# Kernel optimization log

Measured on AMD Instinct MI355X. Metric: run time of the kernel, lower is better.

## Reference

```python
import jax, jax.numpy as jnp
import numpy as np
from jax import lax


def setup_inputs() -> dict:
    key = jax.random.key(0)
    k1, k2 = jax.random.split(key)
    B, T, C = 8, 4096, 256
    UNITS, WINDOW = 256, 2
    x = jax.random.normal(k1, (B, T, C), dtype=jnp.float32)
    kernel = jax.random.normal(k2, (WINDOW, C, 3 * UNITS), dtype=jnp.float32) * 0.05
    bias = jnp.zeros((3 * UNITS,), dtype=jnp.float32)
    return {"x": x, "kernel": kernel, "bias": bias}


def _qrnn_forward(x, kernel, bias):
    # Causal conv1d: left-pad time axis by (window - 1).
    window = kernel.shape[0]
    xp = jnp.pad(x, ((0, 0), (window - 1, 0), (0, 0)))
    gates = lax.conv_general_dilated(
        xp, kernel, window_strides=(1,), padding='VALID',
        dimension_numbers=('NWC', 'WIO', 'NWC')) + bias
    z, f, o = jnp.split(gates, 3, axis=-1)  # each [B, T, units]
    z = jnp.tanh(z)
    f = jax.nn.sigmoid(f)

    # fo_pool: c_t = f_t * c_{t-1} + (1 - f_t) * z_t, c_0 = 0.
    # Linear recurrence -> associative scan over time with elements (a, b):
    # compose((a1,b1),(a2,b2)) = (a1*a2, a2*b1 + b2).
    def combine(e1, e2):
        a1, b1 = e1
        a2, b2 = e2
        return a1 * a2, a2 * b1 + b2

    _, c = lax.associative_scan(combine, (f, (1.0 - f) * z), axis=1)
    h = jax.nn.sigmoid(o) * c  # output gate
    return h  # return_sequences=True -> [B, T, units]


def reference(x, kernel, bias):
    return _qrnn_forward(x, kernel, bias)
```

## Files before the change

kernel.cpp:

```cpp
#include <hip/hip_runtime.h>
#include <math.h>


#define Bq 8
#define Tq 4096
#define NCq 64
#define Lq 64

typedef __attribute__((ext_vector_type(8))) _Float16 f16x8;
typedef __attribute__((ext_vector_type(4))) float f32x4;

__device__ __forceinline__ float sigmoidf_(float x) {
    return 1.f / (1.f + __expf(-x));
}
__device__ __forceinline__ float tanh_fast(float x) {
    return 1.f - 2.f / (__expf(2.f * x) + 1.f);
}
__device__ __forceinline__ unsigned short f16b(float a) {
    _Float16 h = (_Float16)a;
    return *(unsigned short*)&h;
}
__device__ __forceinline__ void gload16(const void* g, void* l) {
    __builtin_amdgcn_global_load_lds(
        (const __attribute__((address_space(1))) void*)g,
        (__attribute__((address_space(3))) void*)l, 16, 0, 0);
}

__global__ __launch_bounds__(256) void split_xk(
    const float* __restrict__ x, const float* __restrict__ kw,
    _Float16* __restrict__ xh, _Float16* __restrict__ bh)
{
    const int NX = Bq * 4097 * 64;
    int idx = blockIdx.x * 256 + threadIdx.x;
    if (idx < NX) {
        int b  = idx / (4097 * 64);
        int r  = idx % (4097 * 64);
        int tp = r / 64, c4 = (r % 64) << 2;
        size_t o = ((size_t)(b * 4097 + tp) << 8) + c4;
        _Float16 h4[4] = {(_Float16)0.f, (_Float16)0.f, (_Float16)0.f, (_Float16)0.f};
        if (tp > 0) {
            const float4 v = *(const float4*)&x[((size_t)(b * 4096 + tp - 1) << 8) + c4];
            h4[0] = (_Float16)v.x; h4[1] = (_Float16)v.y;
            h4[2] = (_Float16)v.z; h4[3] = (_Float16)v.w;
        }
        *(ushort4*)&xh[o] = *(ushort4*)h4;
    } else {
        int j = idx - NX;
        if (j < 768 * 512) {
            int n = j >> 9, k = j & 511;
            bh[((size_t)n << 9) + k] = (_Float16)kw[(size_t)k * 768 + n];
        }
    }
}

__global__ __launch_bounds__(256) void conv_gemm(
    const _Float16* __restrict__ xh, const _Float16* __restrict__ bth,
    const float* __restrict__ bias,
    _Float16* __restrict__ Z, _Float16* __restrict__ G, _Float16* __restrict__ SO)
{
    __shared__ __align__(16) char smem[65536];
    const int tid = threadIdx.x;
    const int l = tid & 63, w = tid >> 6;
    const int wr = w >> 1, wc = w & 1;
    const int bm = blockIdx.x;
    const int by = blockIdx.y;
    const int b  = bm >> 5;
    const int t0 = (bm & 31) << 7;
    const int n0 = by << 7;

    f32x4 acc[4][4] = {};

    const int rowT   = tid >> 2;
    const int slotSw = (tid & 3) ^ ((rowT >> 1) & 3);
    size_t gaBase = ((size_t)(b * 4097 + t0 + rowT) << 8) + (slotSw << 3);
    size_t gbBase = ((size_t)(n0 + rowT) << 9) + (slotSw << 3);
    const int ldsW = w << 9;

    int offA[4], offB[4];
    const int colB = (l >> 4) << 4;
    #pragma unroll
    for (int i = 0; i < 4; ++i) {
        int ra = wr * 64 + i * 16 + (l & 15);
        offA[i] = ((ra << 6) + colB) ^ (((ra >> 1) & 3) << 4);
        int rb = wc * 64 + i * 16 + (l & 15);
        offB[i] = ((rb << 6) + colB) ^ (((rb >> 1) & 3) << 4);
    }

    auto stage = [&](int kk) {
        const int buf = kk & 3;
        _Float16* pA = (_Float16*)(smem + buf * 16384) + ldsW;
        _Float16* pB = (_Float16*)(smem + buf * 16384 + 8192) + ldsW;
        size_t ga = gaBase + (size_t)kk * 32;
        size_t gb = gbBase + (size_t)kk * 32;
        gload16(xh  + ga,          pA);
        gload16(xh  + ga + 16384,  pA + 2048);
        gload16(bth + gb,          pB);
        gload16(bth + gb + 32768,  pB + 2048);
    };

    auto compute = [&](int kk) {
        const char* bA = (const char*)smem + (kk & 3) * 16384;
        const char* bB = bA + 8192;
        f16x8 fa[4], fb[4];
        #pragma unroll
        for (int i = 0; i < 4; ++i) {
            fa[i] = *(const f16x8*)(bA + offA[i]);
            fb[i] = *(const f16x8*)(bB + offB[i]);
        }
        __builtin_amdgcn_s_setprio(1);
        #pragma unroll
        for (int mi = 0; mi < 4; ++mi)
            #pragma unroll
            for (int ni = 0; ni < 4; ++ni)
                acc[mi][ni] = __builtin_amdgcn_mfma_f32_16x16x32_f16(
                    fa[mi], fb[ni], acc[mi][ni], 0, 0, 0);
        __builtin_amdgcn_s_setprio(0);
    };

    stage(0);
    stage(1);
#define QSTEP(k, V) \
    if ((k) + 2 < 16) stage((k) + 2); \
    asm volatile("s_waitcnt vmcnt(" #V ")" ::: "memory"); \
    __builtin_amdgcn_s_barrier(); \
    compute(k);
    QSTEP(0, 8)  QSTEP(1, 8)  QSTEP(2, 8)  QSTEP(3, 8)
    QSTEP(4, 8)  QSTEP(5, 8)  QSTEP(6, 8)  QSTEP(7, 8)
    QSTEP(8, 8)  QSTEP(9, 8)  QSTEP(10, 8) QSTEP(11, 8)
    QSTEP(12, 8) QSTEP(13, 8) QSTEP(14, 4) QSTEP(15, 0)
#undef QSTEP
    __syncthreads();

    const int gsel = by >> 1;
    float bb[4];
    #pragma unroll
    for (int ni = 0; ni < 4; ++ni)
        bb[ni] = bias[n0 + wc * 64 + ni * 16 + (l & 15)];

    unsigned short* Hd = (unsigned short*)smem;
    #pragma unroll
    for (int ni = 0; ni < 4; ++ni) {
        const int cl = wc * 64 + ni * 16 + (l & 15);
        #pragma unroll
        for (int mi = 0; mi < 4; ++mi)
            #pragma unroll
            for (int r = 0; r < 4; ++r) {
                const int trl = wr * 64 + mi * 16 + ((l >> 4) << 2) + r;
                float g = acc[mi][ni][r] + bb[ni];
                float a = (gsel == 0) ? tanh_fast(g)
                        : (gsel == 1) ? sigmoidf_(-g)
                                      : sigmoidf_(g);
                int byt = (trl << 8) + ((cl << 1) ^ (((trl >> 2) & 3) << 4));
                *(unsigned short*)((char*)Hd + byt) = f16b(a);
            }
    }
    __syncthreads();
    _Float16* Gg = (gsel == 0) ? Z : (gsel == 1) ? G : SO;
    const int u0 = n0 & 255;
    const size_t gbase = ((size_t)(b * 4096 + t0) << 8) + u0;
    #pragma unroll
    for (int j = 0; j < 8; ++j) {
        int hoff = tid * 8 + j * 2048;
        int row  = hoff >> 7;
        int cby  = (hoff & 127) << 1;
        int srcB = (row << 8) + (cby ^ (((row >> 2) & 3) << 4));
        int4 v = *(const int4*)((const char*)Hd + srcB);
        *(int4*)&Gg[gbase + ((size_t)row << 8) + (cby >> 1)] = v;
    }
}

__global__ __launch_bounds__(256) void chunk_reduce(
    const _Float16* __restrict__ Z, const _Float16* __restrict__ G,
    float* __restrict__ CA, float* __restrict__ CB)
{
    const int u = threadIdx.x;
    const int blk = blockIdx.x;
    const int b = blk >> 6, ck = blk & 63;
    size_t base = (((size_t)b << 12) + ck * Lq) * 256 + u;
    float A = 1.f, Bv = 0.f;
    #pragma unroll 8
    for (int s = 0; s < Lq; ++s) {
        size_t idx = base + (size_t)s * 256;
        float g = (float)G[idx];
        float z = (float)Z[idx];
        Bv = fmaf(1.f - g, Bv, g * z);
        A *= (1.f - g);
    }
    size_t cidx = ((size_t)b * NCq + ck) * 256 + u;
    CA[cidx] = A;
    CB[cidx] = Bv;
}

__global__ __launch_bounds__(256) void carry_scan(
    const float* __restrict__ CA, const float* __restrict__ CB,
    float* __restrict__ CIN)
{
    const int u = threadIdx.x;
    const int b = blockIdx.x;
    float c = 0.f;
    #pragma unroll 8
    for (int k = 0; k < NCq; ++k) {
        size_t idx = ((size_t)b * NCq + k) * 256 + u;
        CIN[idx] = c;
        c = fmaf(CA[idx], c, CB[idx]);
    }
}

__global__ __launch_bounds__(256) void apply_scan(
    const _Float16* __restrict__ Z, const _Float16* __restrict__ G,
    const _Float16* __restrict__ SO, const float* __restrict__ CIN,
    float* __restrict__ out)
{
    const int u = threadIdx.x;
    const int blk = blockIdx.x;
    const int b = blk >> 6, ck = blk & 63;
    float c = CIN[((size_t)b * NCq + ck) * 256 + u];
    size_t base = (((size_t)b << 12) + ck * Lq) * 256 + u;
    #pragma unroll 8
    for (int s = 0; s < Lq; ++s) {
        size_t idx = base + (size_t)s * 256;
        float g = (float)G[idx], z = (float)Z[idx];
        c = fmaf(1.f - g, c, g * z);
        out[idx] = (float)SO[idx] * c;
    }
}

extern "C" void kernel_launch(void* const* d_in, const int* in_sizes, int n_in,
                              void* d_out, int out_size, void* d_ws, size_t ws_size,
                              hipStream_t stream) {
    const float* x    = (const float*)d_in[0];
    const float* kw   = (const float*)d_in[1];
    const float* bias = (const float*)d_in[2];
    float* out = (float*)d_out;

    char* p = (char*)d_ws;
    _Float16* xh  = (_Float16*)p; p += (size_t)Bq * 4097 * 256 * 2;
    _Float16* bth = (_Float16*)p; p += (size_t)768 * 512 * 2;
    _Float16* Z   = (_Float16*)p; p += (size_t)Bq * Tq * 256 * 2;
    _Float16* G   = (_Float16*)p; p += (size_t)Bq * Tq * 256 * 2;
    _Float16* SO  = (_Float16*)p; p += (size_t)Bq * Tq * 256 * 2;
    float* CA  = (float*)p; p += (size_t)Bq * NCq * 256 * 4;
    float* CB  = (float*)p; p += (size_t)Bq * NCq * 256 * 4;
    float* CIN = (float*)p;

    const int NX = Bq * 4097 * 64;
    split_xk<<<(NX + 768 * 512 + 255) / 256, 256, 0, stream>>>(x, kw, xh, bth);
    dim3 g1(256, 6);
    conv_gemm<<<g1, 256, 0, stream>>>(xh, bth, bias, Z, G, SO);
    chunk_reduce<<<512, 256, 0, stream>>>(Z, G, CA, CB);
    carry_scan<<<Bq, 256, 0, stream>>>(CA, CB, CIN);
    apply_scan<<<512, 256, 0, stream>>>(Z, G, SO, CIN, out);
}
```

Measured before the change: 90.84 us.

## Widen conv GEMM tile to 128x256 with double-buffered LDS pipeline

The conv GEMM block tile grows from 128x128 to 128x256 outputs, so each block computes one full gate (z, f or o) and the grid shrinks from 256x6 to 256x3. The 4-stage global_load_lds pipeline with vmcnt waits is replaced by a simple 2-buffer scheme with __syncthreads, and launch bounds now request 2 blocks per CU. The aim is more reuse of A tiles and fewer redundant A loads. In exchange, per-thread accumulators double, there are fewer blocks (768), and the shallower pipeline hides less load latency.

```diff
diff --git a/kernel.cpp b/kernel.cpp
--- a/kernel.cpp
+++ b/kernel.cpp
@@ -53,7 +53,7 @@
     }
 }
 
-__global__ __launch_bounds__(256) void conv_gemm(
+__global__ __launch_bounds__(256, 2) void conv_gemm(
     const _Float16* __restrict__ xh, const _Float16* __restrict__ bth,
     const float* __restrict__ bias,
     _Float16* __restrict__ Z, _Float16* __restrict__ G, _Float16* __restrict__ SO)
@@ -62,109 +62,108 @@
     const int tid = threadIdx.x;
     const int l = tid & 63, w = tid >> 6;
     const int wr = w >> 1, wc = w & 1;
+    const int lg = l >> 4, l15 = l & 15;
     const int bm = blockIdx.x;
     const int by = blockIdx.y;
     const int b  = bm >> 5;
     const int t0 = (bm & 31) << 7;
-    const int n0 = by << 7;
-
-    f32x4 acc[4][4] = {};
+    const int n0 = by << 8;
+
+    f32x4 acc[4][8] = {};
 
     const int rowT   = tid >> 2;
     const int slotSw = (tid & 3) ^ ((rowT >> 1) & 3);
     size_t gaBase = ((size_t)(b * 4097 + t0 + rowT) << 8) + (slotSw << 3);
     size_t gbBase = ((size_t)(n0 + rowT) << 9) + (slotSw << 3);
-    const int ldsW = w << 9;
-
-    int offA[4], offB[4];
-    const int colB = (l >> 4) << 4;
+    const int ldsW = w << 10;
+
+    int offA[4], offB[8];
     #pragma unroll
     for (int i = 0; i < 4; ++i) {
-        int ra = wr * 64 + i * 16 + (l & 15);
-        offA[i] = ((ra << 6) + colB) ^ (((ra >> 1) & 3) << 4);
-        int rb = wc * 64 + i * 16 + (l & 15);
-        offB[i] = ((rb << 6) + colB) ^ (((rb >> 1) & 3) << 4);
-    }
-
-    auto stage = [&](int kk) {
-        const int buf = kk & 3;
-        _Float16* pA = (_Float16*)(smem + buf * 16384) + ldsW;
-        _Float16* pB = (_Float16*)(smem + buf * 16384 + 8192) + ldsW;
+        int ra = wr * 64 + i * 16 + l15;
+        offA[i] = ((ra << 6) + (lg << 4)) ^ (((ra >> 1) & 3) << 4);
+    }
+    #pragma unroll
+    for (int i = 0; i < 8; ++i) {
+        int rb = wc * 128 + i * 16 + l15;
+        offB[i] = ((rb << 6) + (lg << 4)) ^ (((rb >> 1) & 3) << 4);
+    }
+
+    auto stage = [&](int buf, int kk) {
+        char* bA = smem + buf * 24576;
+        char* bB = bA + 8192;
         size_t ga = gaBase + (size_t)kk * 32;
         size_t gb = gbBase + (size_t)kk * 32;
-        gload16(xh  + ga,          pA);
-        gload16(xh  + ga + 16384,  pA + 2048);
-        gload16(bth + gb,          pB);
-        gload16(bth + gb + 32768,  pB + 2048);
+        #pragma unroll
+        for (int g = 0; g < 2; ++g)
+            gload16(xh + ga + (size_t)g * 16384, bA + g * 4096 + ldsW);
+        #pragma unroll
+        for (int g = 0; g < 4; ++g)
+            gload16(bth + gb + (size_t)g * 32768, bB + g * 4096 + ldsW);
     };
 
-    auto compute = [&](int kk) {
-        const char* bA = (const char*)smem + (kk & 3) * 16384;
+    auto compute = [&](int buf) {
+        const char* bA = smem + buf * 24576;
         const char* bB = bA + 8192;
-        f16x8 fa[4], fb[4];
-        #pragma unroll
-        for (int i = 0; i < 4; ++i) {
-            fa[i] = *(const f16x8*)(bA + offA[i]);
-            fb[i] = *(const f16x8*)(bB + offB[i]);
-        }
+        f16x8 fa[4], fb[8];
+        #pragma unroll
+        for (int i = 0; i < 4; ++i) fa[i] = *(const f16x8*)(bA + offA[i]);
+        #pragma unroll
+        for (int i = 0; i < 8; ++i) fb[i] = *(const f16x8*)(bB + offB[i]);
         __builtin_amdgcn_s_setprio(1);
         #pragma unroll
         for (int mi = 0; mi < 4; ++mi)
             #pragma unroll
-            for (int ni = 0; ni < 4; ++ni)
+            for (int ni = 0; ni < 8; ++ni)
                 acc[mi][ni] = __builtin_amdgcn_mfma_f32_16x16x32_f16(
                     fa[mi], fb[ni], acc[mi][ni], 0, 0, 0);
         __builtin_amdgcn_s_setprio(0);
     };
 
-    stage(0);
-    stage(1);
-#define QSTEP(k, V) \
-    if ((k) + 2 < 16) stage((k) + 2); \
-    asm volatile("s_waitcnt vmcnt(" #V ")" ::: "memory"); \
-    __builtin_amdgcn_s_barrier(); \
-    compute(k);
-    QSTEP(0, 8)  QSTEP(1, 8)  QSTEP(2, 8)  QSTEP(3, 8)
-    QSTEP(4, 8)  QSTEP(5, 8)  QSTEP(6, 8)  QSTEP(7, 8)
-    QSTEP(8, 8)  QSTEP(9, 8)  QSTEP(10, 8) QSTEP(11, 8)
-    QSTEP(12, 8) QSTEP(13, 8) QSTEP(14, 4) QSTEP(15, 0)
-#undef QSTEP
+    stage(0, 0);
     __syncthreads();
-
-    const int gsel = by >> 1;
-    float bb[4];
-    #pragma unroll
-    for (int ni = 0; ni < 4; ++ni)
-        bb[ni] = bias[n0 + wc * 64 + ni * 16 + (l & 15)];
+    int buf = 0;
+    #pragma unroll
+    for (int kk = 0; kk < 16; ++kk) {
+        if (kk < 15) stage(buf ^ 1, kk + 1);
+        compute(buf);
+        __syncthreads();
+        buf ^= 1;
+    }
+
+    const int gsel = by;
+    float bb[8];
+    #pragma unroll
+    for (int ni = 0; ni < 8; ++ni)
+        bb[ni] = bias[n0 + wc * 128 + ni * 16 + l15];
 
     unsigned short* Hd = (unsigned short*)smem;
     #pragma unroll
-    for (int ni = 0; ni < 4; ++ni) {
-        const int cl = wc * 64 + ni * 16 + (l & 15);
+    for (int ni = 0; ni < 8; ++ni) {
+        const int cl = wc * 128 + ni * 16 + l15;
         #pragma unroll
         for (int mi = 0; mi < 4; ++mi)
             #pragma unroll
             for (int r = 0; r < 4; ++r) {
-                const int trl = wr * 64 + mi * 16 + ((l >> 4) << 2) + r;
+                const int trl = wr * 64 + mi * 16 + lg * 4 + r;
                 float g = acc[mi][ni][r] + bb[ni];
                 float a = (gsel == 0) ? tanh_fast(g)
                         : (gsel == 1) ? sigmoidf_(-g)
                                       : sigmoidf_(g);
-                int byt = (trl << 8) + ((cl << 1) ^ (((trl >> 2) & 3) << 4));
+                int byt = (trl << 9) + ((cl << 1) ^ (((trl >> 2) & 3) << 4));
                 *(unsigned short*)((char*)Hd + byt) = f16b(a);
             }
     }
     __syncthreads();
     _Float16* Gg = (gsel == 0) ? Z : (gsel == 1) ? G : SO;
-    const int u0 = n0 & 255;
-    const size_t gbase = ((size_t)(b * 4096 + t0) << 8) + u0;
-    #pragma unroll
-    for (int j = 0; j < 8; ++j) {
-        int hoff = tid * 8 + j * 2048;
-        int row  = hoff >> 7;
-        int cby  = (hoff & 127) << 1;
-        int srcB = (row << 8) + (cby ^ (((row >> 2) & 3) << 4));
-        int4 v = *(const int4*)((const char*)Hd + srcB);
+    const size_t gbase = ((size_t)(b * 4096 + t0)) << 8;
+    #pragma unroll
+    for (int i = 0; i < 16; ++i) {
+        int off = (i * 256 + tid) << 4;
+        int row = off >> 9;
+        int cby = off & 511;
+        int src = (row << 9) + (cby ^ (((row >> 2) & 3) << 4));
+        int4 v = *(const int4*)((const char*)Hd + src);
         *(int4*)&Gg[gbase + ((size_t)row << 8) + (cby >> 1)] = v;
     }
 }
@@ -245,7 +244,7 @@
 
     const int NX = Bq * 4097 * 64;
     split_xk<<<(NX + 768 * 512 + 255) / 256, 256, 0, stream>>>(x, kw, xh, bth);
-    dim3 g1(256, 6);
+    dim3 g1(256, 3);
     conv_gemm<<<g1, 256, 0, stream>>>(xh, bth, bias, Z, G, SO);
     chunk_reduce<<<512, 256, 0, stream>>>(Z, G, CA, CB);
     carry_scan<<<Bq, 256, 0, stream>>>(CA, CB, CIN);
```

New measurement: 100.8 us. +11.0%, slower.

## Switch conv GEMM to 32x32x16 MFMA with double-buffered LDS pipeline

Applied to the files above, without the earlier changes.

Replaces the 16x16x32 MFMA tiling (4x4 accumulators per wave) with 32x32x16 MFMA tiles (2x2 accumulators), changing the LDS fragment addressing and epilogue index mapping to match. The four-stage LDS ring with explicit vmcnt waits is replaced by a simpler two-buffer loop with a full __syncthreads per k-step, halving shared memory. Larger MFMA tiles mean fewer LDS fragment reads per FLOP, and the smaller LDS footprint may allow more resident blocks. The price is less prefetch depth, an extra barrier per iteration, and dropping the setprio hints, so global load latency may be less well hidden.

```diff
diff --git a/kernel.cpp b/kernel.cpp
--- a/kernel.cpp
+++ b/kernel.cpp
@@ -8,7 +8,7 @@
 #define Lq 64
 
 typedef __attribute__((ext_vector_type(8))) _Float16 f16x8;
-typedef __attribute__((ext_vector_type(4))) float f32x4;
+typedef __attribute__((ext_vector_type(16))) float f32x16;
 
 __device__ __forceinline__ float sigmoidf_(float x) {
     return 1.f / (1.f + __expf(-x));
@@ -58,17 +58,18 @@
     const float* __restrict__ bias,
     _Float16* __restrict__ Z, _Float16* __restrict__ G, _Float16* __restrict__ SO)
 {
-    __shared__ __align__(16) char smem[65536];
+    __shared__ __align__(16) char smem[32768];
     const int tid = threadIdx.x;
     const int l = tid & 63, w = tid >> 6;
     const int wr = w >> 1, wc = w & 1;
+    const int l31 = l & 31, lh = l >> 5;
     const int bm = blockIdx.x;
     const int by = blockIdx.y;
     const int b  = bm >> 5;
     const int t0 = (bm & 31) << 7;
     const int n0 = by << 7;
 
-    f32x4 acc[4][4] = {};
+    f32x16 acc[2][2] = {};
 
     const int rowT   = tid >> 2;
     const int slotSw = (tid & 3) ^ ((rowT >> 1) & 3);
@@ -76,20 +77,21 @@
     size_t gbBase = ((size_t)(n0 + rowT) << 9) + (slotSw << 3);
     const int ldsW = w << 9;
 
-    int offA[4], offB[4];
-    const int colB = (l >> 4) << 4;
-    #pragma unroll
-    for (int i = 0; i < 4; ++i) {
-        int ra = wr * 64 + i * 16 + (l & 15);
-        offA[i] = ((ra << 6) + colB) ^ (((ra >> 1) & 3) << 4);
-        int rb = wc * 64 + i * 16 + (l & 15);
-        offB[i] = ((rb << 6) + colB) ^ (((rb >> 1) & 3) << 4);
-    }
-
-    auto stage = [&](int kk) {
-        const int buf = kk & 3;
-        _Float16* pA = (_Float16*)(smem + buf * 16384) + ldsW;
-        _Float16* pB = (_Float16*)(smem + buf * 16384 + 8192) + ldsW;
+    int offA[2][2], offB[2][2];
+    #pragma unroll
+    for (int i = 0; i < 2; ++i) {
+        int ra = wr * 64 + i * 32 + l31;
+        int rb = wc * 64 + i * 32 + l31;
+        #pragma unroll
+        for (int kh = 0; kh < 2; ++kh) {
+            offA[i][kh] = (ra << 6) + ((((kh << 1) + lh) ^ ((ra >> 1) & 3)) << 4);
+            offB[i][kh] = (rb << 6) + ((((kh << 1) + lh) ^ ((rb >> 1) & 3)) << 4);
+        }
+    }
+
+    auto stage = [&](int buf, int kk) {
+        _Float16* pA = (_Float16*)smem + buf * 8192 + ldsW;
+        _Float16* pB = pA + 4096;
         size_t ga = gaBase + (size_t)kk * 32;
         size_t gb = gbBase + (size_t)kk * 32;
         gload16(xh  + ga,          pA);
@@ -98,55 +100,54 @@
         gload16(bth + gb + 32768,  pB + 2048);
     };
 
-    auto compute = [&](int kk) {
-        const char* bA = (const char*)smem + (kk & 3) * 16384;
+    auto compute = [&](int buf) {
+        const char* bA = (const char*)smem + buf * 16384;
         const char* bB = bA + 8192;
-        f16x8 fa[4], fb[4];
-        #pragma unroll
-        for (int i = 0; i < 4; ++i) {
-            fa[i] = *(const f16x8*)(bA + offA[i]);
-            fb[i] = *(const f16x8*)(bB + offB[i]);
-        }
-        __builtin_amdgcn_s_setprio(1);
-        #pragma unroll
-        for (int mi = 0; mi < 4; ++mi)
+        f16x8 fa[2][2], fb[2][2];
+        #pragma unroll
+        for (int i = 0; i < 2; ++i)
             #pragma unroll
-            for (int ni = 0; ni < 4; ++ni)
-                acc[mi][ni] = __builtin_amdgcn_mfma_f32_16x16x32_f16(
-                    fa[mi], fb[ni], acc[mi][ni], 0, 0, 0);
-        __builtin_amdgcn_s_setprio(0);
+            for (int kh = 0; kh < 2; ++kh) {
+                fa[i][kh] = *(const f16x8*)(bA + offA[i][kh]);
+                fb[i][kh] = *(const f16x8*)(bB + offB[i][kh]);
+            }
+        #pragma unroll
+        for (int mi = 0; mi < 2; ++mi)
+            #pragma unroll
+            for (int ni = 0; ni < 2; ++ni)
+                #pragma unroll
+                for (int kh = 0; kh < 2; ++kh)
+                    acc[mi][ni] = __builtin_amdgcn_mfma_f32_32x32x16_f16(
+                        fa[mi][kh], fb[ni][kh], acc[mi][ni], 0, 0, 0);
     };
 
-    stage(0);
-    stage(1);
-#define QSTEP(k, V) \
-    if ((k) + 2 < 16) stage((k) + 2); \
-    asm volatile("s_waitcnt vmcnt(" #V ")" ::: "memory"); \
-    __builtin_amdgcn_s_barrier(); \
-    compute(k);
-    QSTEP(0, 8)  QSTEP(1, 8)  QSTEP(2, 8)  QSTEP(3, 8)
-    QSTEP(4, 8)  QSTEP(5, 8)  QSTEP(6, 8)  QSTEP(7, 8)
-    QSTEP(8, 8)  QSTEP(9, 8)  QSTEP(10, 8) QSTEP(11, 8)
-    QSTEP(12, 8) QSTEP(13, 8) QSTEP(14, 4) QSTEP(15, 0)
-#undef QSTEP
+    stage(0, 0);
     __syncthreads();
+    int buf = 0;
+    #pragma unroll
+    for (int kk = 0; kk < 16; ++kk) {
+        if (kk < 15) stage(buf ^ 1, kk + 1);
+        compute(buf);
+        __syncthreads();
+        buf ^= 1;
+    }
 
     const int gsel = by >> 1;
-    float bb[4];
-    #pragma unroll
-    for (int ni = 0; ni < 4; ++ni)
-        bb[ni] = bias[n0 + wc * 64 + ni * 16 + (l & 15)];
+    float bb[2];
+    #pragma unroll
+    for (int ni = 0; ni < 2; ++ni)
+        bb[ni] = bias[n0 + wc * 64 + ni * 32 + l31];
 
     unsigned short* Hd = (unsigned short*)smem;
     #pragma unroll
-    for (int ni = 0; ni < 4; ++ni) {
-        const int cl = wc * 64 + ni * 16 + (l & 15);
-        #pragma unroll
-        for (int mi = 0; mi < 4; ++mi)
+    for (int ni = 0; ni < 2; ++ni) {
+        const int cl = wc * 64 + ni * 32 + l31;
+        #pragma unroll
+        for (int mi = 0; mi < 2; ++mi)
             #pragma unroll
-            for (int r = 0; r < 4; ++r) {
-                const int trl = wr * 64 + mi * 16 + ((l >> 4) << 2) + r;
-                float g = acc[mi][ni][r] + bb[ni];
+            for (int q = 0; q < 16; ++q) {
+                const int trl = wr * 64 + mi * 32 + (q & 3) + ((q >> 2) << 3) + (lh << 2);
+                float g = acc[mi][ni][q] + bb[ni];
                 float a = (gsel == 0) ? tanh_fast(g)
                         : (gsel == 1) ? sigmoidf_(-g)
                                       : sigmoidf_(g);
```

Measured after the change: 89.09 us. Within noise of the previous version (-1.9%).
